# Optimization experiments

Hardware: AMD Instinct MI355X
Metric: run time of the kernel (lower is better)

## Reference

```python
import jax, jax.numpy as jnp
import numpy as np

NODE_DIM = 512
PROMPT_DIM = 512
N_NODES = 100000
N_GRAPHS = 1024


def setup_inputs() -> dict:
    key = jax.random.key(0)
    k1, k2, k3, k4, k5, k6, k7 = jax.random.split(key, 7)
    node_feats = jax.random.normal(k1, (N_NODES, NODE_DIM), dtype=jnp.float32)
    graph_prompt = jax.random.normal(k2, (N_GRAPHS, PROMPT_DIM), dtype=jnp.float32)
    batch_idx = jnp.sort(jax.random.randint(k3, (N_NODES,), 0, N_GRAPHS))
    # Linear init ~ U(-1/sqrt(fan_in), 1/sqrt(fan_in)) like torch defaults
    fan1 = NODE_DIM + PROMPT_DIM
    b1 = 1.0 / np.sqrt(fan1)
    W1 = jax.random.uniform(k4, (fan1, NODE_DIM), minval=-b1, maxval=b1, dtype=jnp.float32)
    bias1 = jax.random.uniform(k5, (NODE_DIM,), minval=-b1, maxval=b1, dtype=jnp.float32)
    b2 = 1.0 / np.sqrt(NODE_DIM)
    W2 = jax.random.uniform(k6, (NODE_DIM, NODE_DIM), minval=-b2, maxval=b2, dtype=jnp.float32)
    bias2 = jax.random.uniform(k7, (NODE_DIM,), minval=-b2, maxval=b2, dtype=jnp.float32)
    return {"node_feats": node_feats, "graph_prompt": graph_prompt, "batch_idx": batch_idx,
            "W1": W1, "bias1": bias1, "W2": W2, "bias2": bias2}


def reference(node_feats, graph_prompt, batch_idx, W1, bias1, W2, bias2):
    # gather per-node prompt: [N, prompt_dim]
    prompt_expanded = graph_prompt[batch_idx]
    combined = jnp.concatenate([node_feats, prompt_expanded], axis=-1)  # [N, node_dim+prompt_dim]
    h = jax.nn.relu(combined @ W1 + bias1)  # [N, node_dim]
    return h @ W2 + bias2  # [N, node_dim]
```

## Files before the change

kernel.cpp:

```cpp
#include <hip/hip_runtime.h>


#define N_NODES   100000

typedef __bf16 bf16x8 __attribute__((ext_vector_type(8)));
typedef float  f32x4  __attribute__((ext_vector_type(4)));
typedef unsigned short ushort_t;

__device__ __forceinline__ ushort_t f2bf(float f) {
  __bf16 b = (__bf16)f;
  return __builtin_bit_cast(unsigned short, b);
}

__device__ __forceinline__ void gload_lds16(const void* g, void* l) {
  __builtin_amdgcn_global_load_lds(
      (const __attribute__((address_space(1))) void*)g,
      (__attribute__((address_space(3))) void*)l, 16, 0, 0);
}

__global__ void prep_kernel(const float* __restrict__ gp, const float* __restrict__ W1,
                            const float* __restrict__ W2, ushort_t* __restrict__ prm,
                            ushort_t* __restrict__ W1T, ushort_t* __restrict__ W2T) {
  int i = blockIdx.x * 256 + threadIdx.x;
  if (i < 524288) {
    prm[i] = f2bf(gp[i]);
  } else if (i < 1048576) {
    int j = i - 524288;
    int n = j >> 10, k = j & 1023;
    W1T[j] = f2bf(W1[k * 512 + n]);
  } else if (i < 1310720) {
    int j = i - 1048576;
    int n = j >> 9, k = j & 511;
    W2T[j] = f2bf(W2[k * 512 + n]);
  }
}

__global__ __launch_bounds__(256, 2) void p2_kernel(
    const ushort_t* __restrict__ prm, const ushort_t* __restrict__ W1T,
    const float* __restrict__ bias1, float* __restrict__ P2) {
  __shared__ ushort_t sA[128 * 64];
  __shared__ ushort_t sB[128 * 64];
  const int tid = threadIdx.x, lane = tid & 63, wid = tid >> 6;
  const int m0 = (blockIdx.x >> 2) * 128, n0 = (blockIdx.x & 3) * 128;

  const ushort_t* pA[4]; const ushort_t* pB[4]; int ldsW[4];
#pragma unroll
  for (int s = 0; s < 4; ++s) {
    int q = wid * 256 + s * 64 + lane;
    int row = q >> 3;
    int cw = (q & 7) ^ (row & 7);
    pA[s] = prm + (size_t)(m0 + row) * 512 + cw * 8;
    pB[s] = W1T + (size_t)(n0 + row) * 1024 + 512 + cw * 8;
    ldsW[s] = (wid * 256 + s * 64) * 8;
  }
  f32x4 acc[4][4];
#pragma unroll
  for (int i = 0; i < 4; ++i)
#pragma unroll
    for (int j = 0; j < 4; ++j) acc[i][j] = {0.f, 0.f, 0.f, 0.f};
  const int wm = (wid >> 1) * 64, wn = (wid & 1) * 64;
  const int lr = lane >> 4, lc = lane & 15;

  for (int kt = 0; kt < 8; ++kt) {
#pragma unroll
    for (int s = 0; s < 4; ++s) {
      gload_lds16(pA[s], &sA[ldsW[s]]); pA[s] += 64;
      gload_lds16(pB[s], &sB[ldsW[s]]); pB[s] += 64;
    }
    __syncthreads();
#pragma unroll
    for (int kk = 0; kk < 2; ++kk) {
      bf16x8 af[4], bfr[4];
#pragma unroll
      for (int i = 0; i < 4; ++i) {
        int row = wm + i * 16 + lc;
        int cp = (kk * 4 + lr) ^ (row & 7);
        af[i] = *(const bf16x8*)&sA[row * 64 + cp * 8];
      }
#pragma unroll
      for (int j = 0; j < 4; ++j) {
        int col = wn + j * 16 + lc;
        int cp = (kk * 4 + lr) ^ (col & 7);
        bfr[j] = *(const bf16x8*)&sB[col * 64 + cp * 8];
      }
#pragma unroll
      for (int i = 0; i < 4; ++i)
#pragma unroll
        for (int j = 0; j < 4; ++j)
          acc[i][j] = __builtin_amdgcn_mfma_f32_16x16x32_bf16(af[i], bfr[j], acc[i][j], 0, 0, 0);
    }
    __syncthreads();
  }
#pragma unroll
  for (int j = 0; j < 4; ++j) {
    int col = n0 + wn + j * 16 + lc;
    float bv = bias1[col];
#pragma unroll
    for (int i = 0; i < 4; ++i)
#pragma unroll
      for (int r = 0; r < 4; ++r) {
        int row = m0 + wm + i * 16 + lr * 4 + r;
        P2[(size_t)row * 512 + col] = acc[i][j][r] + bv;
      }
  }
}

__global__ __launch_bounds__(512, 4) void fused_kernel(
    const float* __restrict__ nf, const int* __restrict__ bidx,
    const ushort_t* __restrict__ W1T, const float* __restrict__ P2,
    const ushort_t* __restrict__ W2T, const float* __restrict__ bias2,
    float* __restrict__ out) {
  __shared__ ushort_t sA[2][64 * 64];
  __shared__ ushort_t sH[64 * 512];

  const int tid = threadIdx.x;
  const int lane = tid & 63;
  const int cg = tid >> 6;
  const int lc = lane & 15, lr = lane >> 4;
  const int m0 = blockIdx.x * 64;

  const int arow = tid >> 3;
  const int aslot = tid & 7;
  const int aclog = aslot ^ (arow & 7);
  int arowg = m0 + arow; if (arowg > N_NODES - 1) arowg = N_NODES - 1;
  const float* abase = nf + (size_t)arowg * 512 + aclog * 8;

  {
    float4 x = *(const float4*)(abase);
    float4 y = *(const float4*)(abase + 4);
    bf16x8 v;
    v[0] = (__bf16)x.x; v[1] = (__bf16)x.y; v[2] = (__bf16)x.z; v[3] = (__bf16)x.w;
    v[4] = (__bf16)y.x; v[5] = (__bf16)y.y; v[6] = (__bf16)y.z; v[7] = (__bf16)y.w;
    *(bf16x8*)&sA[0][tid * 8] = v;
  }
  __syncthreads();

  f32x4 hacc[4][4];
#pragma unroll
  for (int i = 0; i < 4; ++i)
#pragma unroll
    for (int j = 0; j < 4; ++j) hacc[i][j] = {0.f, 0.f, 0.f, 0.f};

#pragma unroll
  for (int kt = 0; kt < 8; ++kt) {
    bf16x8 b1[2][4];
#pragma unroll
    for (int kk = 0; kk < 2; ++kk)
#pragma unroll
      for (int j = 0; j < 4; ++j)
        b1[kk][j] = *(const bf16x8*)(W1T + (size_t)(cg * 64 + j * 16 + lc) * 1024
                                     + kt * 64 + kk * 32 + lr * 8);
    float4 ax, ay;
    if (kt < 7) {
      ax = *(const float4*)(abase + (kt + 1) * 64);
      ay = *(const float4*)(abase + (kt + 1) * 64 + 4);
    }
    const ushort_t* buf = sA[kt & 1];
#pragma unroll
    for (int kk = 0; kk < 2; ++kk) {
#pragma unroll
      for (int i = 0; i < 4; ++i) {
        int row = i * 16 + lc;
        int phys = (kk * 4 + lr) ^ (row & 7);
        bf16x8 a = *(const bf16x8*)&buf[row * 64 + phys * 8];
#pragma unroll
        for (int j = 0; j < 4; ++j)
          hacc[i][j] = __builtin_amdgcn_mfma_f32_16x16x32_bf16(a, b1[kk][j], hacc[i][j], 0, 0, 0);
      }
    }
    if (kt < 7) {
      bf16x8 v;
      v[0] = (__bf16)ax.x; v[1] = (__bf16)ax.y; v[2] = (__bf16)ax.z; v[3] = (__bf16)ax.w;
      v[4] = (__bf16)ay.x; v[5] = (__bf16)ay.y; v[6] = (__bf16)ay.z; v[7] = (__bf16)ay.w;
      *(bf16x8*)&sA[(kt + 1) & 1][tid * 8] = v;
      __syncthreads();
    }
  }

#pragma unroll
  for (int i = 0; i < 4; ++i) {
#pragma unroll
    for (int r = 0; r < 4; ++r) {
      int row = i * 16 + lr * 4 + r;
      int rowg = m0 + row; if (rowg > N_NODES - 1) rowg = N_NODES - 1;
      int g = bidx[rowg];
      const float* p2row = P2 + (size_t)g * 512;
#pragma unroll
      for (int j = 0; j < 4; ++j) {
        int col = cg * 64 + j * 16 + lc;
        float v = fmaxf(hacc[i][j][r] + p2row[col], 0.f);
        int c = col >> 3;
        int phys = (c & 48) | ((c ^ row) & 15);
        *(__bf16*)((char*)sH + row * 1024 + phys * 16 + (col & 7) * 2) = (__bf16)v;
      }
    }
  }
  __syncthreads();

  f32x4 oacc[4][4];
#pragma unroll
  for (int i = 0; i < 4; ++i)
#pragma unroll
    for (int j = 0; j < 4; ++j) oacc[i][j] = {0.f, 0.f, 0.f, 0.f};

#pragma unroll
  for (int kk = 0; kk < 16; ++kk) {
    int kl = kk * 32 + lr * 8;
    bf16x8 a2[4];
#pragma unroll
    for (int i = 0; i < 4; ++i) {
      int row = i * 16 + lc;
      int c = kk * 4 + lr;
      int phys = (c & 48) | ((c ^ row) & 15);
      a2[i] = *(const bf16x8*)&sH[row * 512 + phys * 8];
    }
#pragma unroll
    for (int j = 0; j < 4; ++j) {
      bf16x8 b2 = *(const bf16x8*)(W2T + (size_t)(cg * 64 + j * 16 + lc) * 512 + kl);
#pragma unroll
      for (int i = 0; i < 4; ++i)
        oacc[i][j] = __builtin_amdgcn_mfma_f32_16x16x32_bf16(a2[i], b2, oacc[i][j], 0, 0, 0);
    }
  }

#pragma unroll
  for (int j = 0; j < 4; ++j) {
    int col = cg * 64 + j * 16 + lc;
    float bv = bias2[col];
#pragma unroll
    for (int i = 0; i < 4; ++i)
#pragma unroll
      for (int r = 0; r < 4; ++r) {
        int rowg = m0 + i * 16 + lr * 4 + r;
        if (rowg < N_NODES)
          out[(size_t)rowg * 512 + col] = oacc[i][j][r] + bv;
      }
  }
}

extern "C" void kernel_launch(void* const* d_in, const int* in_sizes, int n_in,
                              void* d_out, int out_size, void* d_ws, size_t ws_size,
                              hipStream_t stream) {
  const float* nf   = (const float*)d_in[0];
  const float* gp   = (const float*)d_in[1];
  const int*   bidx = (const int*)d_in[2];
  const float* W1   = (const float*)d_in[3];
  const float* b1   = (const float*)d_in[4];
  const float* W2   = (const float*)d_in[5];
  const float* b2   = (const float*)d_in[6];
  float* out = (float*)d_out;

  char* ws = (char*)d_ws;
  ushort_t* prm = (ushort_t*)ws;
  ushort_t* W1T = (ushort_t*)(ws + 1048576);
  ushort_t* W2T = (ushort_t*)(ws + 2097152);
  float*    P2  = (float*)   (ws + 2621440);

  prep_kernel<<<5120, 256, 0, stream>>>(gp, W1, W2, prm, W1T, W2T);
  p2_kernel<<<32, 256, 0, stream>>>(prm, W1T, b1, P2);
  fused_kernel<<<(N_NODES + 63) / 64, 512, 0, stream>>>(nf, bidx, W1T, P2, W2T, b2, out);
}
```

Before: 310.8 us.

## Preload P2 into accumulators, double-buffer W1 fragments, use non-draining barriers

Result: slower. 352.7 us (+13.5%).

```diff
diff --git a/kernel.cpp b/kernel.cpp
--- a/kernel.cpp
+++ b/kernel.cpp
@@ -16,6 +16,12 @@
   __builtin_amdgcn_global_load_lds(
       (const __attribute__((address_space(1))) void*)g,
       (__attribute__((address_space(3))) void*)l, 16, 0, 0);
+}
+
+__device__ __forceinline__ void barrier_nodrain() {
+  asm volatile("s_waitcnt lgkmcnt(0)" ::: "memory");
+  __builtin_amdgcn_s_barrier();
+  __builtin_amdgcn_sched_barrier(0);
 }
 
 __global__ void prep_kernel(const float* __restrict__ gp, const float* __restrict__ W1,
@@ -105,7 +111,7 @@
   }
 }
 
-__global__ __launch_bounds__(512, 4) void fused_kernel(
+__global__ __launch_bounds__(512, 2) void fused_kernel(
     const float* __restrict__ nf, const int* __restrict__ bidx,
     const ushort_t* __restrict__ W1T, const float* __restrict__ P2,
     const ushort_t* __restrict__ W2T, const float* __restrict__ bias2,
@@ -120,8 +126,7 @@
   const int m0 = blockIdx.x * 64;
 
   const int arow = tid >> 3;
-  const int aslot = tid & 7;
-  const int aclog = aslot ^ (arow & 7);
+  const int aclog = (tid & 7) ^ (arow & 7);
   int arowg = m0 + arow; if (arowg > N_NODES - 1) arowg = N_NODES - 1;
   const float* abase = nf + (size_t)arowg * 512 + aclog * 8;
 
@@ -133,47 +138,70 @@
     v[4] = (__bf16)y.x; v[5] = (__bf16)y.y; v[6] = (__bf16)y.z; v[7] = (__bf16)y.w;
     *(bf16x8*)&sA[0][tid * 8] = v;
   }
-  __syncthreads();
-
-  f32x4 hacc[4][4];
-#pragma unroll
-  for (int i = 0; i < 4; ++i)
-#pragma unroll
-    for (int j = 0; j < 4; ++j) hacc[i][j] = {0.f, 0.f, 0.f, 0.f};
+
+  f32x4 acc[4][4];
+#pragma unroll
+  for (int i = 0; i < 4; ++i) {
+#pragma unroll
+    for (int r = 0; r < 4; ++r) {
+      int rowg = m0 + i * 16 + lr * 4 + r;
+      if (rowg > N_NODES - 1) rowg = N_NODES - 1;
+      int g = bidx[rowg];
+      const float* p2r = P2 + (size_t)g * 512 + cg * 64 + lc;
+#pragma unroll
+      for (int j = 0; j < 4; ++j) acc[i][j][r] = p2r[j * 16];
+    }
+  }
+
+  const ushort_t* wbase = W1T + (size_t)(cg * 64 + lc) * 1024 + lr * 8;
+  bf16x8 bcur[4];
+#pragma unroll
+  for (int j = 0; j < 4; ++j)
+    bcur[j] = *(const bf16x8*)(wbase + (size_t)j * 16384);
+
+  barrier_nodrain();
 
 #pragma unroll
   for (int kt = 0; kt < 8; ++kt) {
-    bf16x8 b1[2][4];
-#pragma unroll
-    for (int kk = 0; kk < 2; ++kk)
-#pragma unroll
-      for (int j = 0; j < 4; ++j)
-        b1[kk][j] = *(const bf16x8*)(W1T + (size_t)(cg * 64 + j * 16 + lc) * 1024
-                                     + kt * 64 + kk * 32 + lr * 8);
     float4 ax, ay;
     if (kt < 7) {
       ax = *(const float4*)(abase + (kt + 1) * 64);
       ay = *(const float4*)(abase + (kt + 1) * 64 + 4);
     }
     const ushort_t* buf = sA[kt & 1];
-#pragma unroll
-    for (int kk = 0; kk < 2; ++kk) {
-#pragma unroll
-      for (int i = 0; i < 4; ++i) {
-        int row = i * 16 + lc;
-        int phys = (kk * 4 + lr) ^ (row & 7);
-        bf16x8 a = *(const bf16x8*)&buf[row * 64 + phys * 8];
-#pragma unroll
-        for (int j = 0; j < 4; ++j)
-          hacc[i][j] = __builtin_amdgcn_mfma_f32_16x16x32_bf16(a, b1[kk][j], hacc[i][j], 0, 0, 0);
-      }
+    bf16x8 bnxt[4];
+#pragma unroll
+    for (int j = 0; j < 4; ++j)
+      bnxt[j] = *(const bf16x8*)(wbase + (size_t)j * 16384 + kt * 64 + 32);
+#pragma unroll
+    for (int i = 0; i < 4; ++i) {
+      int row = i * 16 + lc;
+      int phys = lr ^ (row & 7);
+      bf16x8 a = *(const bf16x8*)&buf[row * 64 + phys * 8];
+#pragma unroll
+      for (int j = 0; j < 4; ++j)
+        acc[i][j] = __builtin_amdgcn_mfma_f32_16x16x32_bf16(a, bcur[j], acc[i][j], 0, 0, 0);
+    }
+    if (kt < 7) {
+#pragma unroll
+      for (int j = 0; j < 4; ++j)
+        bcur[j] = *(const bf16x8*)(wbase + (size_t)j * 16384 + (kt + 1) * 64);
+    }
+#pragma unroll
+    for (int i = 0; i < 4; ++i) {
+      int row = i * 16 + lc;
+      int phys = (4 + lr) ^ (row & 7);
+      bf16x8 a = *(const bf16x8*)&buf[row * 64 + phys * 8];
+#pragma unroll
+      for (int j = 0; j < 4; ++j)
+        acc[i][j] = __builtin_amdgcn_mfma_f32_16x16x32_bf16(a, bnxt[j], acc[i][j], 0, 0, 0);
     }
     if (kt < 7) {
       bf16x8 v;
       v[0] = (__bf16)ax.x; v[1] = (__bf16)ax.y; v[2] = (__bf16)ax.z; v[3] = (__bf16)ax.w;
       v[4] = (__bf16)ay.x; v[5] = (__bf16)ay.y; v[6] = (__bf16)ay.z; v[7] = (__bf16)ay.w;
       *(bf16x8*)&sA[(kt + 1) & 1][tid * 8] = v;
-      __syncthreads();
+      barrier_nodrain();
     }
   }
 
@@ -182,44 +210,39 @@
 #pragma unroll
     for (int r = 0; r < 4; ++r) {
       int row = i * 16 + lr * 4 + r;
-      int rowg = m0 + row; if (rowg > N_NODES - 1) rowg = N_NODES - 1;
-      int g = bidx[rowg];
-      const float* p2row = P2 + (size_t)g * 512;
 #pragma unroll
       for (int j = 0; j < 4; ++j) {
         int col = cg * 64 + j * 16 + lc;
-        float v = fmaxf(hacc[i][j][r] + p2row[col], 0.f);
+        float v = fmaxf(acc[i][j][r], 0.f);
         int c = col >> 3;
         int phys = (c & 48) | ((c ^ row) & 15);
         *(__bf16*)((char*)sH + row * 1024 + phys * 16 + (col & 7) * 2) = (__bf16)v;
       }
     }
   }
-  __syncthreads();
-
-  f32x4 oacc[4][4];
+  barrier_nodrain();
+
 #pragma unroll
   for (int i = 0; i < 4; ++i)
 #pragma unroll
-    for (int j = 0; j < 4; ++j) oacc[i][j] = {0.f, 0.f, 0.f, 0.f};
-
+    for (int j = 0; j < 4; ++j) acc[i][j] = {0.f, 0.f, 0.f, 0.f};
+
+  const ushort_t* w2base = W2T + (size_t)(cg * 64 + lc) * 512 + lr * 8;
 #pragma unroll
   for (int kk = 0; kk < 16; ++kk) {
-    int kl = kk * 32 + lr * 8;
-    bf16x8 a2[4];
+    bf16x8 b2f[4];
+#pragma unroll
+    for (int j = 0; j < 4; ++j)
+      b2f[j] = *(const bf16x8*)(w2base + (size_t)j * 8192 + kk * 32);
 #pragma unroll
     for (int i = 0; i < 4; ++i) {
       int row = i * 16 + lc;
       int c = kk * 4 + lr;
       int phys = (c & 48) | ((c ^ row) & 15);
-      a2[i] = *(const bf16x8*)&sH[row * 512 + phys * 8];
-    }
-#pragma unroll
-    for (int j = 0; j < 4; ++j) {
-      bf16x8 b2 = *(const bf16x8*)(W2T + (size_t)(cg * 64 + j * 16 + lc) * 512 + kl);
-#pragma unroll
-      for (int i = 0; i < 4; ++i)
-        oacc[i][j] = __builtin_amdgcn_mfma_f32_16x16x32_bf16(a2[i], b2, oacc[i][j], 0, 0, 0);
+      bf16x8 a2 = *(const bf16x8*)&sH[row * 512 + phys * 8];
+#pragma unroll
+      for (int j = 0; j < 4; ++j)
+        acc[i][j] = __builtin_amdgcn_mfma_f32_16x16x32_bf16(a2, b2f[j], acc[i][j], 0, 0, 0);
     }
   }
 
@@ -233,7 +256,7 @@
       for (int r = 0; r < 4; ++r) {
         int rowg = m0 + i * 16 + lr * 4 + r;
         if (rowg < N_NODES)
-          out[(size_t)rowg * 512 + col] = oacc[i][j][r] + bv;
+          out[(size_t)rowg * 512 + col] = acc[i][j][r] + bv;
       }
   }
 }
```

## Split fused MLP into two LDS-free GEMM kernels with bf16 hidden buffer

Applied to the files above, without the earlier changes.

Result: slower. 679.6 us (+118.6%).

```diff
diff --git a/kernel.cpp b/kernel.cpp
--- a/kernel.cpp
+++ b/kernel.cpp
@@ -1,7 +1,7 @@
 #include <hip/hip_runtime.h>
 
 
-#define N_NODES   100000
+#define N_NODES 100000
 
 typedef __bf16 bf16x8 __attribute__((ext_vector_type(8)));
 typedef float  f32x4  __attribute__((ext_vector_type(4)));
@@ -12,230 +12,201 @@
   return __builtin_bit_cast(unsigned short, b);
 }
 
-__device__ __forceinline__ void gload_lds16(const void* g, void* l) {
-  __builtin_amdgcn_global_load_lds(
-      (const __attribute__((address_space(1))) void*)g,
-      (__attribute__((address_space(3))) void*)l, 16, 0, 0);
-}
-
-__global__ void prep_kernel(const float* __restrict__ gp, const float* __restrict__ W1,
-                            const float* __restrict__ W2, ushort_t* __restrict__ prm,
+__device__ __forceinline__ bf16x8 cvt8(const float* p) {
+  float4 x = *(const float4*)p;
+  float4 y = *(const float4*)(p + 4);
+  bf16x8 v;
+  v[0] = (__bf16)x.x; v[1] = (__bf16)x.y; v[2] = (__bf16)x.z; v[3] = (__bf16)x.w;
+  v[4] = (__bf16)y.x; v[5] = (__bf16)y.y; v[6] = (__bf16)y.z; v[7] = (__bf16)y.w;
+  return v;
+}
+
+__device__ __forceinline__ int xcd_swizzle(int orig, int nwg) {
+  int q = nwg >> 3, r = nwg & 7;
+  int xcd = orig & 7, pos = orig >> 3;
+  return (xcd < r ? xcd * (q + 1) : r * (q + 1) + (xcd - r) * q) + pos;
+}
+
+__global__ void prep_kernel(const float* __restrict__ W1, const float* __restrict__ W2,
                             ushort_t* __restrict__ W1T, ushort_t* __restrict__ W2T) {
   int i = blockIdx.x * 256 + threadIdx.x;
   if (i < 524288) {
-    prm[i] = f2bf(gp[i]);
-  } else if (i < 1048576) {
+    int n = i >> 10, k = i & 1023;
+    W1T[i] = f2bf(W1[k * 512 + n]);
+  } else if (i < 786432) {
     int j = i - 524288;
-    int n = j >> 10, k = j & 1023;
-    W1T[j] = f2bf(W1[k * 512 + n]);
-  } else if (i < 1310720) {
-    int j = i - 1048576;
     int n = j >> 9, k = j & 511;
     W2T[j] = f2bf(W2[k * 512 + n]);
   }
 }
 
-__global__ __launch_bounds__(256, 2) void p2_kernel(
-    const ushort_t* __restrict__ prm, const ushort_t* __restrict__ W1T,
+__global__ __launch_bounds__(256, 4) void p2_kernel(
+    const float* __restrict__ gp, const ushort_t* __restrict__ W1T,
     const float* __restrict__ bias1, float* __restrict__ P2) {
-  __shared__ ushort_t sA[128 * 64];
-  __shared__ ushort_t sB[128 * 64];
   const int tid = threadIdx.x, lane = tid & 63, wid = tid >> 6;
-  const int m0 = (blockIdx.x >> 2) * 128, n0 = (blockIdx.x & 3) * 128;
-
-  const ushort_t* pA[4]; const ushort_t* pB[4]; int ldsW[4];
-#pragma unroll
-  for (int s = 0; s < 4; ++s) {
-    int q = wid * 256 + s * 64 + lane;
-    int row = q >> 3;
-    int cw = (q & 7) ^ (row & 7);
-    pA[s] = prm + (size_t)(m0 + row) * 512 + cw * 8;
-    pB[s] = W1T + (size_t)(n0 + row) * 1024 + 512 + cw * 8;
-    ldsW[s] = (wid * 256 + s * 64) * 8;
-  }
-  f32x4 acc[4][4];
-#pragma unroll
-  for (int i = 0; i < 4; ++i)
+  const int lc = lane & 15, lr = lane >> 4;
+  const int mt = blockIdx.x >> 1, nt = blockIdx.x & 1;
+  const int m0 = mt * 32;
+  const int col0 = nt * 256 + wid * 64;
+
+  f32x4 acc[2][4];
+#pragma unroll
+  for (int i = 0; i < 2; ++i)
 #pragma unroll
     for (int j = 0; j < 4; ++j) acc[i][j] = {0.f, 0.f, 0.f, 0.f};
-  const int wm = (wid >> 1) * 64, wn = (wid & 1) * 64;
-  const int lr = lane >> 4, lc = lane & 15;
-
+
+  const float* a0 = gp + (size_t)(m0 + lc) * 512;
+  const ushort_t* bb = W1T + (size_t)(col0 + lc) * 1024 + 512;
+
+#pragma unroll 2
   for (int kt = 0; kt < 8; ++kt) {
-#pragma unroll
-    for (int s = 0; s < 4; ++s) {
-      gload_lds16(pA[s], &sA[ldsW[s]]); pA[s] += 64;
-      gload_lds16(pB[s], &sB[ldsW[s]]); pB[s] += 64;
+    bf16x8 bfr[2][4];
+#pragma unroll
+    for (int kk = 0; kk < 2; ++kk)
+#pragma unroll
+      for (int j = 0; j < 4; ++j)
+        bfr[kk][j] = *(const bf16x8*)(bb + (size_t)j * 16 * 1024 + kt * 64 + kk * 32 + lr * 8);
+    bf16x8 af[2][2];
+#pragma unroll
+    for (int i = 0; i < 2; ++i)
+#pragma unroll
+      for (int kk = 0; kk < 2; ++kk)
+        af[i][kk] = cvt8(a0 + (size_t)i * 16 * 512 + kt * 64 + kk * 32 + lr * 8);
+#pragma unroll
+    for (int kk = 0; kk < 2; ++kk)
+#pragma unroll
+      for (int i = 0; i < 2; ++i)
+#pragma unroll
+        for (int j = 0; j < 4; ++j)
+          acc[i][j] = __builtin_amdgcn_mfma_f32_16x16x32_bf16(af[i][kk], bfr[kk][j], acc[i][j], 0, 0, 0);
+  }
+
+#pragma unroll
+  for (int i = 0; i < 2; ++i)
+#pragma unroll
+    for (int r = 0; r < 4; ++r) {
+      int row = m0 + i * 16 + lr * 4 + r;
+#pragma unroll
+      for (int j = 0; j < 4; ++j) {
+        int col = col0 + j * 16 + lc;
+        P2[(size_t)row * 512 + col] = acc[i][j][r] + bias1[col];
+      }
     }
-    __syncthreads();
-#pragma unroll
-    for (int kk = 0; kk < 2; ++kk) {
-      bf16x8 af[4], bfr[4];
-#pragma unroll
-      for (int i = 0; i < 4; ++i) {
-        int row = wm + i * 16 + lc;
-        int cp = (kk * 4 + lr) ^ (row & 7);
-        af[i] = *(const bf16x8*)&sA[row * 64 + cp * 8];
-      }
-#pragma unroll
-      for (int j = 0; j < 4; ++j) {
-        int col = wn + j * 16 + lc;
-        int cp = (kk * 4 + lr) ^ (col & 7);
-        bfr[j] = *(const bf16x8*)&sB[col * 64 + cp * 8];
-      }
-#pragma unroll
-      for (int i = 0; i < 4; ++i)
-#pragma unroll
-        for (int j = 0; j < 4; ++j)
-          acc[i][j] = __builtin_amdgcn_mfma_f32_16x16x32_bf16(af[i], bfr[j], acc[i][j], 0, 0, 0);
-    }
-    __syncthreads();
-  }
-#pragma unroll
-  for (int j = 0; j < 4; ++j) {
-    int col = n0 + wn + j * 16 + lc;
-    float bv = bias1[col];
-#pragma unroll
-    for (int i = 0; i < 4; ++i)
-#pragma unroll
-      for (int r = 0; r < 4; ++r) {
-        int row = m0 + wm + i * 16 + lr * 4 + r;
-        P2[(size_t)row * 512 + col] = acc[i][j][r] + bv;
-      }
-  }
-}
-
-__global__ __launch_bounds__(512, 4) void fused_kernel(
+}
+
+__global__ __launch_bounds__(256, 4) void g1_kernel(
     const float* __restrict__ nf, const int* __restrict__ bidx,
     const ushort_t* __restrict__ W1T, const float* __restrict__ P2,
-    const ushort_t* __restrict__ W2T, const float* __restrict__ bias2,
-    float* __restrict__ out) {
-  __shared__ ushort_t sA[2][64 * 64];
-  __shared__ ushort_t sH[64 * 512];
-
-  const int tid = threadIdx.x;
-  const int lane = tid & 63;
-  const int cg = tid >> 6;
+    ushort_t* __restrict__ h) {
+  const int nwg = 6250;
+  const int wg = xcd_swizzle(blockIdx.x, nwg);
+  const int mt = wg >> 1, nt = wg & 1;
+  const int tid = threadIdx.x, lane = tid & 63, wid = tid >> 6;
   const int lc = lane & 15, lr = lane >> 4;
-  const int m0 = blockIdx.x * 64;
-
-  const int arow = tid >> 3;
-  const int aslot = tid & 7;
-  const int aclog = aslot ^ (arow & 7);
-  int arowg = m0 + arow; if (arowg > N_NODES - 1) arowg = N_NODES - 1;
-  const float* abase = nf + (size_t)arowg * 512 + aclog * 8;
-
-  {
-    float4 x = *(const float4*)(abase);
-    float4 y = *(const float4*)(abase + 4);
-    bf16x8 v;
-    v[0] = (__bf16)x.x; v[1] = (__bf16)x.y; v[2] = (__bf16)x.z; v[3] = (__bf16)x.w;
-    v[4] = (__bf16)y.x; v[5] = (__bf16)y.y; v[6] = (__bf16)y.z; v[7] = (__bf16)y.w;
-    *(bf16x8*)&sA[0][tid * 8] = v;
-  }
-  __syncthreads();
-
-  f32x4 hacc[4][4];
-#pragma unroll
-  for (int i = 0; i < 4; ++i)
-#pragma unroll
-    for (int j = 0; j < 4; ++j) hacc[i][j] = {0.f, 0.f, 0.f, 0.f};
-
-#pragma unroll
+  const int m0 = mt * 32;
+  const int col0 = nt * 256 + wid * 64;
+
+  f32x4 acc[2][4];
+#pragma unroll
+  for (int i = 0; i < 2; ++i)
+#pragma unroll
+    for (int j = 0; j < 4; ++j) acc[i][j] = {0.f, 0.f, 0.f, 0.f};
+
+  const float* a0 = nf + (size_t)(m0 + lc) * 512;
+  const ushort_t* bb = W1T + (size_t)(col0 + lc) * 1024;
+
+#pragma unroll 2
   for (int kt = 0; kt < 8; ++kt) {
-    bf16x8 b1[2][4];
+    bf16x8 bfr[2][4];
 #pragma unroll
     for (int kk = 0; kk < 2; ++kk)
 #pragma unroll
       for (int j = 0; j < 4; ++j)
-        b1[kk][j] = *(const bf16x8*)(W1T + (size_t)(cg * 64 + j * 16 + lc) * 1024
-                                     + kt * 64 + kk * 32 + lr * 8);
-    float4 ax, ay;
-    if (kt < 7) {
-      ax = *(const float4*)(abase + (kt + 1) * 64);
-      ay = *(const float4*)(abase + (kt + 1) * 64 + 4);
-    }
-    const ushort_t* buf = sA[kt & 1];
-#pragma unroll
-    for (int kk = 0; kk < 2; ++kk) {
-#pragma unroll
-      for (int i = 0; i < 4; ++i) {
-        int row = i * 16 + lc;
-        int phys = (kk * 4 + lr) ^ (row & 7);
-        bf16x8 a = *(const bf16x8*)&buf[row * 64 + phys * 8];
+        bfr[kk][j] = *(const bf16x8*)(bb + (size_t)j * 16 * 1024 + kt * 64 + kk * 32 + lr * 8);
+    bf16x8 af[2][2];
+#pragma unroll
+    for (int i = 0; i < 2; ++i)
+#pragma unroll
+      for (int kk = 0; kk < 2; ++kk)
+        af[i][kk] = cvt8(a0 + (size_t)i * 16 * 512 + kt * 64 + kk * 32 + lr * 8);
+#pragma unroll
+    for (int kk = 0; kk < 2; ++kk)
+#pragma unroll
+      for (int i = 0; i < 2; ++i)
 #pragma unroll
         for (int j = 0; j < 4; ++j)
-          hacc[i][j] = __builtin_amdgcn_mfma_f32_16x16x32_bf16(a, b1[kk][j], hacc[i][j], 0, 0, 0);
+          acc[i][j] = __builtin_amdgcn_mfma_f32_16x16x32_bf16(af[i][kk], bfr[kk][j], acc[i][j], 0, 0, 0);
+  }
+
+#pragma unroll
+  for (int i = 0; i < 2; ++i)
+#pragma unroll
+    for (int r = 0; r < 4; ++r) {
+      int row = m0 + i * 16 + lr * 4 + r;
+      int g = bidx[row];
+      const float* p2r = P2 + (size_t)g * 512 + col0;
+#pragma unroll
+      for (int j = 0; j < 4; ++j) {
+        float v = fmaxf(acc[i][j][r] + p2r[j * 16 + lc], 0.f);
+        h[(size_t)row * 512 + col0 + j * 16 + lc] = f2bf(v);
       }
     }
-    if (kt < 7) {
-      bf16x8 v;
-      v[0] = (__bf16)ax.x; v[1] = (__bf16)ax.y; v[2] = (__bf16)ax.z; v[3] = (__bf16)ax.w;
-      v[4] = (__bf16)ay.x; v[5] = (__bf16)ay.y; v[6] = (__bf16)ay.z; v[7] = (__bf16)ay.w;
-      *(bf16x8*)&sA[(kt + 1) & 1][tid * 8] = v;
-      __syncthreads();
-    }
-  }
-
-#pragma unroll
-  for (int i = 0; i < 4; ++i) {
+}
+
+__global__ __launch_bounds__(256, 4) void g2_kernel(
+    const ushort_t* __restrict__ h, const ushort_t* __restrict__ W2T,
+    const float* __restrict__ bias2, float* __restrict__ out) {
+  const int nwg = 6250;
+  const int wg = xcd_swizzle(blockIdx.x, nwg);
+  const int mt = wg >> 1, nt = wg & 1;
+  const int tid = threadIdx.x, lane = tid & 63, wid = tid >> 6;
+  const int lc = lane & 15, lr = lane >> 4;
+  const int m0 = mt * 32;
+  const int col0 = nt * 256 + wid * 64;
+
+  f32x4 acc[2][4];
+#pragma unroll
+  for (int i = 0; i < 2; ++i)
+#pragma unroll
+    for (int j = 0; j < 4; ++j) acc[i][j] = {0.f, 0.f, 0.f, 0.f};
+
+  const ushort_t* a0 = h + (size_t)(m0 + lc) * 512;
+  const ushort_t* bb = W2T + (size_t)(col0 + lc) * 512;
+
+#pragma unroll 2
+  for (int kt = 0; kt < 8; ++kt) {
+    bf16x8 bfr[2][4];
+#pragma unroll
+    for (int kk = 0; kk < 2; ++kk)
+#pragma unroll
+      for (int j = 0; j < 4; ++j)
+        bfr[kk][j] = *(const bf16x8*)(bb + (size_t)j * 16 * 512 + kt * 64 + kk * 32 + lr * 8);
+    bf16x8 af[2][2];
+#pragma unroll
+    for (int i = 0; i < 2; ++i)
+#pragma unroll
+      for (int kk = 0; kk < 2; ++kk)
+        af[i][kk] = *(const bf16x8*)(a0 + (size_t)i * 16 * 512 + kt * 64 + kk * 32 + lr * 8);
+#pragma unroll
+    for (int kk = 0; kk < 2; ++kk)
+#pragma unroll
+      for (int i = 0; i < 2; ++i)
+#pragma unroll
+        for (int j = 0; j < 4; ++j)
+          acc[i][j] = __builtin_amdgcn_mfma_f32_16x16x32_bf16(af[i][kk], bfr[kk][j], acc[i][j], 0, 0, 0);
+  }
+
+#pragma unroll
+  for (int i = 0; i < 2; ++i)
 #pragma unroll
     for (int r = 0; r < 4; ++r) {
-      int row = i * 16 + lr * 4 + r;
-      int rowg = m0 + row; if (rowg > N_NODES - 1) rowg = N_NODES - 1;
-      int g = bidx[rowg];
-      const float* p2row = P2 + (size_t)g * 512;
+      int row = m0 + i * 16 + lr * 4 + r;
 #pragma unroll
       for (int j = 0; j < 4; ++j) {
-        int col = cg * 64 + j * 16 + lc;
-        float v = fmaxf(hacc[i][j][r] + p2row[col], 0.f);
-        int c = col >> 3;
-        int phys = (c & 48) | ((c ^ row) & 15);
-        *(__bf16*)((char*)sH + row * 1024 + phys * 16 + (col & 7) * 2) = (__bf16)v;
+        int col = col0 + j * 16 + lc;
+        out[(size_t)row * 512 + col] = acc[i][j][r] + bias2[col];
       }
     }
-  }
-  __syncthreads();
-
-  f32x4 oacc[4][4];
-#pragma unroll
-  for (int i = 0; i < 4; ++i)
-#pragma unroll
-    for (int j = 0; j < 4; ++j) oacc[i][j] = {0.f, 0.f, 0.f, 0.f};
-
-#pragma unroll
-  for (int kk = 0; kk < 16; ++kk) {
-    int kl = kk * 32 + lr * 8;
-    bf16x8 a2[4];
-#pragma unroll
-    for (int i = 0; i < 4; ++i) {
-      int row = i * 16 + lc;
-      int c = kk * 4 + lr;
-      int phys = (c & 48) | ((c ^ row) & 15);
-      a2[i] = *(const bf16x8*)&sH[row * 512 + phys * 8];
-    }
-#pragma unroll
-    for (int j = 0; j < 4; ++j) {
-      bf16x8 b2 = *(const bf16x8*)(W2T + (size_t)(cg * 64 + j * 16 + lc) * 512 + kl);
-#pragma unroll
-      for (int i = 0; i < 4; ++i)
-        oacc[i][j] = __builtin_amdgcn_mfma_f32_16x16x32_bf16(a2[i], b2, oacc[i][j], 0, 0, 0);
-    }
-  }
-
-#pragma unroll
-  for (int j = 0; j < 4; ++j) {
-    int col = cg * 64 + j * 16 + lc;
-    float bv = bias2[col];
-#pragma unroll
-    for (int i = 0; i < 4; ++i)
-#pragma unroll
-      for (int r = 0; r < 4; ++r) {
-        int rowg = m0 + i * 16 + lr * 4 + r;
-        if (rowg < N_NODES)
-          out[(size_t)rowg * 512 + col] = oacc[i][j][r] + bv;
-      }
-  }
 }
 
 extern "C" void kernel_launch(void* const* d_in, const int* in_sizes, int n_in,
@@ -251,12 +222,13 @@
   float* out = (float*)d_out;
 
   char* ws = (char*)d_ws;
-  ushort_t* prm = (ushort_t*)ws;
-  ushort_t* W1T = (ushort_t*)(ws + 1048576);
-  ushort_t* W2T = (ushort_t*)(ws + 2097152);
-  float*    P2  = (float*)   (ws + 2621440);
-
-  prep_kernel<<<5120, 256, 0, stream>>>(gp, W1, W2, prm, W1T, W2T);
-  p2_kernel<<<32, 256, 0, stream>>>(prm, W1T, b1, P2);
-  fused_kernel<<<(N_NODES + 63) / 64, 512, 0, stream>>>(nf, bidx, W1T, P2, W2T, b2, out);
-}
+  ushort_t* W1T = (ushort_t*)ws;
+  ushort_t* W2T = (ushort_t*)(ws + 1048576);
+  float*    P2  = (float*)   (ws + 1572864);
+  ushort_t* hbf = (ushort_t*)(ws + 3670016);
+
+  prep_kernel<<<3072, 256, 0, stream>>>(W1, W2, W1T, W2T);
+  p2_kernel<<<64, 256, 0, stream>>>(gp, W1T, b1, P2);
+  g1_kernel<<<6250, 256, 0, stream>>>(nf, bidx, W1T, P2, hbf);
+  g2_kernel<<<6250, 256, 0, stream>>>(hbf, W2T, b2, out);
+}
```
